# Performance work log

Measured on AMD Instinct MI355X. Metric: run time of the kernel, lower is better.

The kernel has to match this reference:

```python
import jax, jax.numpy as jnp
import numpy as np


def setup_inputs() -> dict:
    key = jax.random.key(0)
    ks = jax.random.split(key, 7)
    B, T, I, H = 32, 2048, 256, 512
    s = 1.0 / np.sqrt(H)
    return {
        "x": jax.random.normal(ks[0], (B, T, I), dtype=jnp.float32),
        "h0": jax.random.normal(ks[1], (1, B, H), dtype=jnp.float32),
        "c0": jax.random.normal(ks[2], (1, B, H), dtype=jnp.float32),
        "W_ih": jax.random.uniform(ks[3], (4 * H, I), dtype=jnp.float32, minval=-s, maxval=s),
        "W_hh": jax.random.uniform(ks[4], (4 * H, H), dtype=jnp.float32, minval=-s, maxval=s),
        "b_ih": jax.random.uniform(ks[5], (4 * H,), dtype=jnp.float32, minval=-s, maxval=s),
        "b_hh": jax.random.uniform(ks[6], (4 * H,), dtype=jnp.float32, minval=-s, maxval=s),
    }


def _lstm(x, h0, c0, W_ih, W_hh, b_ih, b_hh):
    # x: [B, T, I] (batch_first). Precompute input projections for all steps.
    H = h0.shape[-1]
    x_tf = jnp.swapaxes(x, 0, 1)                       # [T, B, I]
    x_gates = jnp.einsum("tbi,gi->tbg", x_tf, W_ih) + b_ih + b_hh  # [T, B, 4H]

    def step(carry, xg):
        h, c = carry
        gates = xg + h @ W_hh.T                        # [B, 4H]
        i_g, f_g, g_g, o_g = jnp.split(gates, 4, axis=-1)  # torch gate order i,f,g,o
        i_g = jax.nn.sigmoid(i_g)
        f_g = jax.nn.sigmoid(f_g)
        g_g = jnp.tanh(g_g)
        o_g = jax.nn.sigmoid(o_g)
        c_new = f_g * c + i_g * g_g
        h_new = o_g * jnp.tanh(c_new)
        return (h_new, c_new), h_new

    (h_f, c_f), hs = jax.lax.scan(step, (h0[0], c0[0]), x_gates)
    result = jnp.swapaxes(hs, 0, 1)                    # [B, T, H] (batch_first)
    return result, (h_f[None], c_f[None])


def reference(x, h0, c0, W_ih, W_hh, b_ih, b_hh):
    return _lstm(x, h0, c0, W_ih, W_hh, b_ih, b_hh)
```

## Files before the change

### kernel.cpp

```cpp
#include <hip/hip_runtime.h>
#include <hip/hip_bf16.h>
#include <stdint.h>


#define B_   32
#define T_   2048
#define I_   256
#define H_   512
#define NB   32
#define NTHR 512
#define JC   16
#define SA   776
#define KSTEPS 24
#define NPAIR (B_ * H_ / 2)

typedef __attribute__((ext_vector_type(8))) short short8;
typedef __attribute__((ext_vector_type(4))) float f32x4;

__device__ __forceinline__ unsigned short f2bf_bits(float v) {
    unsigned int u = __builtin_bit_cast(unsigned int, v);
    unsigned int r = (u + 0x7FFFu + ((u >> 16) & 1u)) >> 16;
    return (unsigned short)r;
}
__device__ __forceinline__ float sigm(float x) {
    return 1.0f / (1.0f + __expf(-x));
}
__device__ __forceinline__ float tanh_fast(float x) {
    float e = __expf(2.0f * x);
    return 1.0f - 2.0f / (e + 1.0f);
}

__global__ void lstm_init(const float* __restrict__ h0,
                          unsigned long long* __restrict__ hbuf0) {
    int i = blockIdx.x * 256 + threadIdx.x;
    if (i < NPAIR) {
        const int b = i >> 8;
        const int c = (i & 255) * 2;
        const unsigned lo = f2bf_bits(h0[b * H_ + c]);
        const unsigned hi = f2bf_bits(h0[b * H_ + c + 1]);
        const unsigned pair = lo | (hi << 16);
        hbuf0[i] = ((unsigned long long)pair << 32) | 0u;
    }
}

__global__ __launch_bounds__(NTHR) void lstm_persistent(
    const float* __restrict__ x,
    const float* __restrict__ c0,
    const float* __restrict__ Wih,
    const float* __restrict__ Whh,
    const float* __restrict__ bih,
    const float* __restrict__ bhh,
    float* __restrict__ out,
    unsigned long long* hbuf)
{
    __shared__ __align__(16) unsigned short Als[B_][SA];
    __shared__ float g_ls[B_][4 * JC + 1];

    const int tid  = threadIdx.x;
    const int bid  = blockIdx.x;
    const int lane = tid & 63;
    const int wave = tid >> 6;
    const int mi   = (wave & 1) * 16;
    const int q    = wave >> 1;
    const int l15  = lane & 15;
    const int kq8  = (lane >> 4) * 8;

    const int grow = q * H_ + bid * JC + l15;
    short8 bfrag[KSTEPS];
#pragma unroll
    for (int s = 0; s < KSTEPS; ++s) {
        const int k0 = s * 32 + kq8;
        short8 f;
#pragma unroll
        for (int j = 0; j < 8; ++j) {
            const int k = k0 + j;
            const float v = (k < H_) ? Whh[(size_t)grow * H_ + k]
                                     : Wih[(size_t)grow * I_ + (k - H_)];
            f[j] = (short)f2bf_bits(v);
        }
        bfrag[s] = f;
    }

    const int eb   = tid >> 4;
    const int ejj  = tid & 15;
    const int ecol = bid * JC + ejj;
    float bias_i = bih[0 * H_ + ecol] + bhh[0 * H_ + ecol];
    float bias_f = bih[1 * H_ + ecol] + bhh[1 * H_ + ecol];
    float bias_g = bih[2 * H_ + ecol] + bhh[2 * H_ + ecol];
    float bias_o = bih[3 * H_ + ecol] + bhh[3 * H_ + ecol];
    float c_reg  = c0[eb * H_ + ecol];

    for (int t = 0; t < T_; ++t) {
        float4 xv[4];
#pragma unroll
        for (int i = 0; i < 4; ++i) {
            const int idx = tid + i * NTHR;
            const int m = idx >> 6, k4 = idx & 63;
            xv[i] = *(const float4*)(x + (size_t)m * T_ * I_ +
                                     (size_t)t * I_ + k4 * 4);
        }
        asm volatile("" ::: "memory");

        const unsigned tt = (unsigned)t;
        unsigned long long* hsrc = hbuf + (size_t)(t & 1) * NPAIR;
        unsigned long long hv[16];
        unsigned need = 0xFFFFu;
        do {
#pragma unroll
            for (int i = 0; i < 16; ++i) {
                if (need & (1u << i)) {
                    hv[i] = __hip_atomic_load(&hsrc[tid + i * NTHR],
                                              __ATOMIC_RELAXED,
                                              __HIP_MEMORY_SCOPE_AGENT);
                }
            }
            unsigned ok = 0;
#pragma unroll
            for (int i = 0; i < 16; ++i)
                if ((unsigned)hv[i] == tt) ok |= (1u << i);
            need &= ~ok;
        } while (need);

#pragma unroll
        for (int i = 0; i < 16; ++i) {
            const int j = tid + i * NTHR;
            const int m = j >> 8;
            const int c = (j & 255) * 2;
            *(unsigned int*)&Als[m][c] = (unsigned int)(hv[i] >> 32);
        }
#pragma unroll
        for (int i = 0; i < 4; ++i) {
            const int idx = tid + i * NTHR;
            const int m = idx >> 6, k4 = idx & 63;
            ushort4 p;
            p.x = f2bf_bits(xv[i].x); p.y = f2bf_bits(xv[i].y);
            p.z = f2bf_bits(xv[i].z); p.w = f2bf_bits(xv[i].w);
            *(ushort4*)&Als[m][H_ + k4 * 4] = p;
        }
        __syncthreads();

        f32x4 acc = {0.f, 0.f, 0.f, 0.f};
        const int mrow = mi + l15;
#pragma unroll
        for (int s = 0; s < KSTEPS; ++s) {
            const short8 a = *(const short8*)&Als[mrow][s * 32 + kq8];
            acc = __builtin_amdgcn_mfma_f32_16x16x32_bf16(a, bfrag[s], acc, 0, 0, 0);
        }
#pragma unroll
        for (int r = 0; r < 4; ++r) {
            g_ls[mi + (lane >> 4) * 4 + r][q * JC + l15] = acc[r];
        }
        __syncthreads();

        const float pi = g_ls[eb][ejj]          + bias_i;
        const float pf = g_ls[eb][JC + ejj]     + bias_f;
        const float pg = g_ls[eb][2 * JC + ejj] + bias_g;
        const float po = g_ls[eb][3 * JC + ejj] + bias_o;
        const float ig = sigm(pi), fg = sigm(pf);
        const float gg = tanh_fast(pg), og = sigm(po);
        c_reg = fg * c_reg + ig * gg;
        const float h = og * tanh_fast(c_reg);

        const unsigned hvb = f2bf_bits(h);
        const unsigned nbv = __shfl_xor(hvb, 1);
        if ((ejj & 1) == 0) {
            const unsigned pair = hvb | (nbv << 16);
            const unsigned long long word =
                ((unsigned long long)pair << 32) | (unsigned)(t + 1);
            __hip_atomic_store(
                &hbuf[(size_t)((t + 1) & 1) * NPAIR + eb * 256 + (ecol >> 1)],
                word, __ATOMIC_RELAXED, __HIP_MEMORY_SCOPE_AGENT);
        }

        out[(size_t)eb * T_ * H_ + (size_t)t * H_ + ecol] = h;
        if (t == T_ - 1) {
            out[(size_t)B_ * T_ * H_ + eb * H_ + ecol] = h;
            out[(size_t)B_ * T_ * H_ + B_ * H_ + eb * H_ + ecol] = c_reg;
        }
    }
}

extern "C" void kernel_launch(void* const* d_in, const int* in_sizes, int n_in,
                              void* d_out, int out_size, void* d_ws, size_t ws_size,
                              hipStream_t stream) {
    const float* x   = (const float*)d_in[0];
    const float* h0  = (const float*)d_in[1];
    const float* c0  = (const float*)d_in[2];
    const float* Wih = (const float*)d_in[3];
    const float* Whh = (const float*)d_in[4];
    const float* bih = (const float*)d_in[5];
    const float* bhh = (const float*)d_in[6];
    float* out = (float*)d_out;

    unsigned long long* hbuf = (unsigned long long*)d_ws;

    hipLaunchKernelGGL(lstm_init, dim3(32), dim3(256), 0, stream, h0, hbuf);
    hipLaunchKernelGGL(lstm_persistent, dim3(NB), dim3(NTHR), 0, stream,
                       x, c0, Wih, Whh, bih, bhh, out, hbuf);
}
```

Measured before the change: 7.145 ms.

## Overlap input-projection MFMAs with h-wait and prefetch x two steps ahead

Splits the shared A tile into a recurrent h part and a double-buffered x part. The x-projection MFMAs now run before the spin-wait on the previous step's h, so input-gate work overlaps with the cross-block synchronisation, and x is prefetched and converted two timesteps ahead. Shared-memory addresses use an XOR swizzle in place of row padding to avoid bank conflicts. The second h buffer is also initialised to a sentinel. This adds a third LDS buffer and more address arithmetic in the critical loop.

```diff
diff --git a/kernel.cpp b/kernel.cpp
--- a/kernel.cpp
+++ b/kernel.cpp
@@ -10,7 +10,6 @@
 #define NB   32
 #define NTHR 512
 #define JC   16
-#define SA   776
 #define KSTEPS 24
 #define NPAIR (B_ * H_ / 2)
 
@@ -31,7 +30,7 @@
 }
 
 __global__ void lstm_init(const float* __restrict__ h0,
-                          unsigned long long* __restrict__ hbuf0) {
+                          unsigned long long* __restrict__ hbuf) {
     int i = blockIdx.x * 256 + threadIdx.x;
     if (i < NPAIR) {
         const int b = i >> 8;
@@ -39,11 +38,12 @@
         const unsigned lo = f2bf_bits(h0[b * H_ + c]);
         const unsigned hi = f2bf_bits(h0[b * H_ + c + 1]);
         const unsigned pair = lo | (hi << 16);
-        hbuf0[i] = ((unsigned long long)pair << 32) | 0u;
-    }
-}
-
-__global__ __launch_bounds__(NTHR) void lstm_persistent(
+        hbuf[i] = ((unsigned long long)pair << 32) | 0u;
+        hbuf[NPAIR + i] = 0xFFFFFFFFull;
+    }
+}
+
+__global__ __launch_bounds__(NTHR, 1) void lstm_persistent(
     const float* __restrict__ x,
     const float* __restrict__ c0,
     const float* __restrict__ Wih,
@@ -53,7 +53,8 @@
     float* __restrict__ out,
     unsigned long long* hbuf)
 {
-    __shared__ __align__(16) unsigned short Als[B_][SA];
+    __shared__ __align__(16) unsigned short Als[B_][512];
+    __shared__ __align__(16) unsigned short Axls[2][B_][256];
     __shared__ float g_ls[B_][4 * JC + 1];
 
     const int tid  = threadIdx.x;
@@ -64,6 +65,7 @@
     const int q    = wave >> 1;
     const int l15  = lane & 15;
     const int kq8  = (lane >> 4) * 8;
+    const int qv   = lane >> 4;
 
     const int grow = q * H_ + bid * JC + l15;
     short8 bfrag[KSTEPS];
@@ -90,22 +92,71 @@
     float bias_o = bih[3 * H_ + ecol] + bhh[3 * H_ + ecol];
     float c_reg  = c0[eb * H_ + ecol];
 
-    for (int t = 0; t < T_; ++t) {
-        float4 xv[4];
+    char* alsb = (char*)&Als[0][0];
+
+    float4 xv[4];
+#pragma unroll
+    for (int i = 0; i < 4; ++i) {
+        const int idx = tid + i * NTHR;
+        const int m = idx >> 6, k4 = idx & 63;
+        xv[i] = *(const float4*)(x + (size_t)m * T_ * I_ + k4 * 4);
+    }
+    {
+        char* axw = (char*)&Axls[0][0][0];
 #pragma unroll
         for (int i = 0; i < 4; ++i) {
             const int idx = tid + i * NTHR;
             const int m = idx >> 6, k4 = idx & 63;
-            xv[i] = *(const float4*)(x + (size_t)m * T_ * I_ +
-                                     (size_t)t * I_ + k4 * 4);
-        }
-        asm volatile("" ::: "memory");
-
+            ushort4 pk;
+            pk.x = f2bf_bits(xv[i].x); pk.y = f2bf_bits(xv[i].y);
+            pk.z = f2bf_bits(xv[i].z); pk.w = f2bf_bits(xv[i].w);
+            const unsigned a = (unsigned)(m * 512) +
+                (((unsigned)(k4 >> 1) ^ (unsigned)(m & 7)) << 4) +
+                (unsigned)((k4 & 1) * 8);
+            *(ushort4*)(axw + a) = pk;
+        }
+    }
+#pragma unroll
+    for (int i = 0; i < 4; ++i) {
+        const int idx = tid + i * NTHR;
+        const int m = idx >> 6, k4 = idx & 63;
+        xv[i] = *(const float4*)(x + (size_t)m * T_ * I_ + (size_t)I_ + k4 * 4);
+    }
+    __syncthreads();
+
+    const int  mrow = mi + l15;
+    const unsigned r7 = (unsigned)(mrow & 7);
+
+    for (int t = 0; t < T_; ++t) {
         const unsigned tt = (unsigned)t;
         unsigned long long* hsrc = hbuf + (size_t)(t & 1) * NPAIR;
+
         unsigned long long hv[16];
-        unsigned need = 0xFFFFu;
-        do {
+#pragma unroll
+        for (int i = 0; i < 16; ++i) {
+            hv[i] = __hip_atomic_load(&hsrc[tid + i * NTHR],
+                                      __ATOMIC_RELAXED,
+                                      __HIP_MEMORY_SCOPE_AGENT);
+        }
+        asm volatile("" ::: "memory");
+
+        f32x4 acc = {0.f, 0.f, 0.f, 0.f};
+        {
+            const char* axb = (const char*)&Axls[t & 1][0][0];
+#pragma unroll
+            for (int s = 0; s < 8; ++s) {
+                const unsigned off = (unsigned)(mrow * 512) +
+                    (((unsigned)(s * 4 + qv) ^ r7) << 4);
+                const short8 a = *(const short8*)(axb + off);
+                acc = __builtin_amdgcn_mfma_f32_16x16x32_bf16(a, bfrag[16 + s], acc, 0, 0, 0);
+            }
+        }
+
+        unsigned need = 0;
+#pragma unroll
+        for (int i = 0; i < 16; ++i)
+            if ((unsigned)hv[i] != tt) need |= (1u << i);
+        while (need) {
 #pragma unroll
             for (int i = 0; i < 16; ++i) {
                 if (need & (1u << i)) {
@@ -119,36 +170,46 @@
             for (int i = 0; i < 16; ++i)
                 if ((unsigned)hv[i] == tt) ok |= (1u << i);
             need &= ~ok;
-        } while (need);
+        }
 
 #pragma unroll
         for (int i = 0; i < 16; ++i) {
-            const int j = tid + i * NTHR;
-            const int m = j >> 8;
-            const int c = (j & 255) * 2;
-            *(unsigned int*)&Als[m][c] = (unsigned int)(hv[i] >> 32);
-        }
-#pragma unroll
-        for (int i = 0; i < 4; ++i) {
-            const int idx = tid + i * NTHR;
-            const int m = idx >> 6, k4 = idx & 63;
-            ushort4 p;
-            p.x = f2bf_bits(xv[i].x); p.y = f2bf_bits(xv[i].y);
-            p.z = f2bf_bits(xv[i].z); p.w = f2bf_bits(xv[i].w);
-            *(ushort4*)&Als[m][H_ + k4 * 4] = p;
+            const int j  = tid + i * NTHR;
+            const int m  = j >> 8;
+            const int cp = j & 255;
+            const unsigned a = (unsigned)(m * 1024) +
+                (((unsigned)(cp >> 2) ^ (unsigned)(m & 7)) << 4) +
+                (unsigned)((cp & 3) * 4);
+            *(unsigned*)(alsb + a) = (unsigned)(hv[i] >> 32);
         }
         __syncthreads();
 
-        f32x4 acc = {0.f, 0.f, 0.f, 0.f};
-        const int mrow = mi + l15;
-#pragma unroll
-        for (int s = 0; s < KSTEPS; ++s) {
-            const short8 a = *(const short8*)&Als[mrow][s * 32 + kq8];
+#pragma unroll
+        for (int s = 0; s < 16; ++s) {
+            const unsigned off = (unsigned)(mrow * 1024) +
+                (((unsigned)(s * 4 + qv) ^ r7) << 4);
+            const short8 a = *(const short8*)(alsb + off);
             acc = __builtin_amdgcn_mfma_f32_16x16x32_bf16(a, bfrag[s], acc, 0, 0, 0);
         }
 #pragma unroll
         for (int r = 0; r < 4; ++r) {
             g_ls[mi + (lane >> 4) * 4 + r][q * JC + l15] = acc[r];
+        }
+
+        {
+            char* axw = (char*)&Axls[(t + 1) & 1][0][0];
+#pragma unroll
+            for (int i = 0; i < 4; ++i) {
+                const int idx = tid + i * NTHR;
+                const int m = idx >> 6, k4 = idx & 63;
+                ushort4 pk;
+                pk.x = f2bf_bits(xv[i].x); pk.y = f2bf_bits(xv[i].y);
+                pk.z = f2bf_bits(xv[i].z); pk.w = f2bf_bits(xv[i].w);
+                const unsigned a = (unsigned)(m * 512) +
+                    (((unsigned)(k4 >> 1) ^ (unsigned)(m & 7)) << 4) +
+                    (unsigned)((k4 & 1) * 8);
+                *(ushort4*)(axw + a) = pk;
+            }
         }
         __syncthreads();
 
@@ -170,6 +231,17 @@
             __hip_atomic_store(
                 &hbuf[(size_t)((t + 1) & 1) * NPAIR + eb * 256 + (ecol >> 1)],
                 word, __ATOMIC_RELAXED, __HIP_MEMORY_SCOPE_AGENT);
+        }
+
+        {
+            const int tn = (t + 2 < T_) ? t + 2 : T_ - 1;
+#pragma unroll
+            for (int i = 0; i < 4; ++i) {
+                const int idx = tid + i * NTHR;
+                const int m = idx >> 6, k4 = idx & 63;
+                xv[i] = *(const float4*)(x + (size_t)m * T_ * I_ +
+                                         (size_t)tn * I_ + k4 * 4);
+            }
         }
 
         out[(size_t)eb * T_ * H_ + (size_t)t * H_ + ecol] = h;
```

New measurement: 10.42 ms. 45.9% more time.

## Precompute input projection in a parallel GEMM before the recurrent loop

Applied to the files above, without the earlier changes.

Adds a separate bf16 MFMA GEMM kernel that computes x·W_ih^T for all timesteps into workspace before the recurrence. The persistent recurrent kernel then only multiplies h by W_hh (16 K-steps instead of 24) and prefetches the precomputed gate inputs for the next step. This takes the x loads, bf16 conversion and input matmul off the serial critical path. In exchange it needs a large workspace buffer (~0.5 GB), falling back to the old fused kernel when the workspace is too small, and adds extra global memory traffic to write and read the precomputed gates.

```diff
diff --git a/kernel.cpp b/kernel.cpp
--- a/kernel.cpp
+++ b/kernel.cpp
@@ -10,9 +10,12 @@
 #define NB   32
 #define NTHR 512
 #define JC   16
+#define KH   16
+#define KSTEPS 24
 #define SA   776
-#define KSTEPS 24
 #define NPAIR (B_ * H_ / 2)
+#define G4H  (4 * H_)
+#define XGSTEP (B_ * G4H)
 
 typedef __attribute__((ext_vector_type(8))) short short8;
 typedef __attribute__((ext_vector_type(4))) float f32x4;
@@ -31,7 +34,8 @@
 }
 
 __global__ void lstm_init(const float* __restrict__ h0,
-                          unsigned long long* __restrict__ hbuf0) {
+                          const float* __restrict__ Wih,
+                          unsigned long long* __restrict__ ws, int big) {
     int i = blockIdx.x * 256 + threadIdx.x;
     if (i < NPAIR) {
         const int b = i >> 8;
@@ -39,19 +43,210 @@
         const unsigned lo = f2bf_bits(h0[b * H_ + c]);
         const unsigned hi = f2bf_bits(h0[b * H_ + c + 1]);
         const unsigned pair = lo | (hi << 16);
-        hbuf0[i] = ((unsigned long long)pair << 32) | 0u;
-    }
-}
-
-__global__ __launch_bounds__(NTHR) void lstm_persistent(
+        ws[i] = ((unsigned long long)pair << 32) | 0u;
+        ws[NPAIR + i] = 0xFFFFFFFFull;
+    }
+    if (big) {
+        unsigned short* Wihb = (unsigned short*)(ws + 2 * (size_t)NPAIR);
+        const int base = i * 64;
+#pragma unroll
+        for (int k = 0; k < 16; ++k) {
+            float4 v = *(const float4*)(Wih + base + k * 4);
+            ushort4 p;
+            p.x = f2bf_bits(v.x); p.y = f2bf_bits(v.y);
+            p.z = f2bf_bits(v.z); p.w = f2bf_bits(v.w);
+            *(ushort4*)(Wihb + base + k * 4) = p;
+        }
+    }
+}
+
+__global__ __launch_bounds__(NTHR) void xg_gemm(
     const float* __restrict__ x,
+    unsigned long long* __restrict__ ws)
+{
+    __shared__ __align__(16) unsigned short Axp[B_][I_];
+
+    const unsigned short* Wihb = (const unsigned short*)(ws + 2 * (size_t)NPAIR);
+    float* xg = (float*)(Wihb + (size_t)G4H * I_);
+
+    const int t    = blockIdx.x;
+    const int tid  = threadIdx.x;
+    const int lane = tid & 63;
+    const int wave = tid >> 6;
+    const int l15  = lane & 15;
+    const int kq8  = (lane >> 4) * 8;
+
+#pragma unroll
+    for (int i = 0; i < 4; ++i) {
+        const int idx = tid + i * NTHR;
+        const int m = idx >> 6, k4 = idx & 63;
+        float4 v = *(const float4*)(x + (size_t)m * T_ * I_ +
+                                    (size_t)t * I_ + k4 * 4);
+        ushort4 pk;
+        pk.x = f2bf_bits(v.x); pk.y = f2bf_bits(v.y);
+        pk.z = f2bf_bits(v.z); pk.w = f2bf_bits(v.w);
+        *(ushort4*)&Axp[m][k4 * 4] = pk;
+    }
+    __syncthreads();
+
+    short8 afr[2][8];
+#pragma unroll
+    for (int mt = 0; mt < 2; ++mt)
+#pragma unroll
+        for (int ks = 0; ks < 8; ++ks)
+            afr[mt][ks] = *(const short8*)&Axp[mt * 16 + l15][ks * 32 + kq8];
+
+    for (int j = 0; j < 16; ++j) {
+        const int n0 = (wave + 8 * j) * 16;
+        short8 bfr[8];
+#pragma unroll
+        for (int ks = 0; ks < 8; ++ks)
+            bfr[ks] = *(const short8*)(Wihb + (size_t)(n0 + l15) * I_ +
+                                       ks * 32 + kq8);
+        f32x4 a0 = {0.f,0.f,0.f,0.f}, a1 = {0.f,0.f,0.f,0.f};
+#pragma unroll
+        for (int ks = 0; ks < 8; ++ks) {
+            a0 = __builtin_amdgcn_mfma_f32_16x16x32_bf16(afr[0][ks], bfr[ks], a0, 0, 0, 0);
+            a1 = __builtin_amdgcn_mfma_f32_16x16x32_bf16(afr[1][ks], bfr[ks], a1, 0, 0, 0);
+        }
+        float* o = xg + (size_t)t * XGSTEP + n0 + l15;
+#pragma unroll
+        for (int r = 0; r < 4; ++r) {
+            o[(size_t)(((lane >> 4) * 4) + r) * G4H]      = a0[r];
+            o[(size_t)(16 + ((lane >> 4) * 4) + r) * G4H] = a1[r];
+        }
+    }
+}
+
+__global__ __launch_bounds__(NTHR, 1) void lstm_rec(
     const float* __restrict__ c0,
-    const float* __restrict__ Wih,
     const float* __restrict__ Whh,
     const float* __restrict__ bih,
     const float* __restrict__ bhh,
     float* __restrict__ out,
-    unsigned long long* hbuf)
+    unsigned long long* ws)
+{
+    __shared__ __align__(16) unsigned short Als[B_][SA];
+    __shared__ float g_ls[B_][4 * JC + 1];
+
+    const unsigned short* Wihb = (const unsigned short*)(ws + 2 * (size_t)NPAIR);
+    const float* xg = (const float*)(Wihb + (size_t)G4H * I_);
+
+    const int tid  = threadIdx.x;
+    const int bid  = blockIdx.x;
+    const int lane = tid & 63;
+    const int wave = tid >> 6;
+    const int mi   = (wave & 1) * 16;
+    const int q    = wave >> 1;
+    const int l15  = lane & 15;
+    const int kq8  = (lane >> 4) * 8;
+
+    const int grow = q * H_ + bid * JC + l15;
+    short8 bfrag[KH];
+#pragma unroll
+    for (int s = 0; s < KH; ++s) {
+        const int k0 = s * 32 + kq8;
+        short8 f;
+#pragma unroll
+        for (int j = 0; j < 8; ++j)
+            f[j] = (short)f2bf_bits(Whh[(size_t)grow * H_ + k0 + j]);
+        bfrag[s] = f;
+    }
+
+    const int eb   = tid >> 4;
+    const int ejj  = tid & 15;
+    const int ecol = bid * JC + ejj;
+    float bias_i = bih[0 * H_ + ecol] + bhh[0 * H_ + ecol];
+    float bias_f = bih[1 * H_ + ecol] + bhh[1 * H_ + ecol];
+    float bias_g = bih[2 * H_ + ecol] + bhh[2 * H_ + ecol];
+    float bias_o = bih[3 * H_ + ecol] + bhh[3 * H_ + ecol];
+    float c_reg  = c0[eb * H_ + ecol];
+
+    const float* xp0 = xg + (size_t)eb * G4H + ecol;
+    float xg0 = xp0[0], xg1 = xp0[H_], xg2 = xp0[2 * H_], xg3 = xp0[3 * H_];
+
+    for (int t = 0; t < T_; ++t) {
+        const unsigned tt = (unsigned)t;
+        unsigned long long* hsrc = ws + (size_t)(t & 1) * NPAIR;
+
+        unsigned long long hv[16];
+        unsigned need = 0xFFFFu;
+        do {
+#pragma unroll
+            for (int i = 0; i < 16; ++i) {
+                if (need & (1u << i)) {
+                    hv[i] = __hip_atomic_load(&hsrc[tid + i * NTHR],
+                                              __ATOMIC_RELAXED,
+                                              __HIP_MEMORY_SCOPE_AGENT);
+                }
+            }
+            unsigned ok = 0;
+#pragma unroll
+            for (int i = 0; i < 16; ++i)
+                if ((unsigned)hv[i] == tt) ok |= (1u << i);
+            need &= ~ok;
+        } while (need);
+
+#pragma unroll
+        for (int i = 0; i < 16; ++i) {
+            const int j = tid + i * NTHR;
+            const int m = j >> 8;
+            const int c = (j & 255) * 2;
+            *(unsigned int*)&Als[m][c] = (unsigned int)(hv[i] >> 32);
+        }
+        __syncthreads();
+
+        f32x4 acc = {0.f, 0.f, 0.f, 0.f};
+        const int mrow = mi + l15;
+#pragma unroll
+        for (int s = 0; s < KH; ++s) {
+            const short8 a = *(const short8*)&Als[mrow][s * 32 + kq8];
+            acc = __builtin_amdgcn_mfma_f32_16x16x32_bf16(a, bfrag[s], acc, 0, 0, 0);
+        }
+#pragma unroll
+        for (int r = 0; r < 4; ++r) {
+            g_ls[mi + (lane >> 4) * 4 + r][q * JC + l15] = acc[r];
+        }
+        __syncthreads();
+
+        const float pi = g_ls[eb][ejj]          + bias_i + xg0;
+        const float pf = g_ls[eb][JC + ejj]     + bias_f + xg1;
+        const float pg = g_ls[eb][2 * JC + ejj] + bias_g + xg2;
+        const float po = g_ls[eb][3 * JC + ejj] + bias_o + xg3;
+        const float ig = sigm(pi), fg = sigm(pf);
+        const float gg = tanh_fast(pg), og = sigm(po);
+        c_reg = fg * c_reg + ig * gg;
+        const float h = og * tanh_fast(c_reg);
+
+        const unsigned hvb = f2bf_bits(h);
+        const unsigned nbv = __shfl_xor(hvb, 1);
+        if ((ejj & 1) == 0) {
+            const unsigned pair = hvb | (nbv << 16);
+            const unsigned long long word =
+                ((unsigned long long)pair << 32) | (unsigned)(t + 1);
+            __hip_atomic_store(
+                &ws[(size_t)((t + 1) & 1) * NPAIR + eb * 256 + (ecol >> 1)],
+                word, __ATOMIC_RELAXED, __HIP_MEMORY_SCOPE_AGENT);
+        }
+
+        if (t + 1 < T_) {
+            const float* p = xg + (size_t)(t + 1) * XGSTEP + eb * G4H + ecol;
+            xg0 = p[0]; xg1 = p[H_]; xg2 = p[2 * H_]; xg3 = p[3 * H_];
+        }
+
+        out[(size_t)eb * T_ * H_ + (size_t)t * H_ + ecol] = h;
+        if (t == T_ - 1) {
+            out[(size_t)B_ * T_ * H_ + eb * H_ + ecol] = h;
+            out[(size_t)B_ * T_ * H_ + B_ * H_ + eb * H_ + ecol] = c_reg;
+        }
+    }
+}
+
+__global__ __launch_bounds__(NTHR) void lstm_fb(
+    const float* __restrict__ x, const float* __restrict__ c0,
+    const float* __restrict__ Wih, const float* __restrict__ Whh,
+    const float* __restrict__ bih, const float* __restrict__ bhh,
+    float* __restrict__ out, unsigned long long* hbuf)
 {
     __shared__ __align__(16) unsigned short Als[B_][SA];
     __shared__ float g_ls[B_][4 * JC + 1];
@@ -192,9 +387,21 @@
     const float* bhh = (const float*)d_in[6];
     float* out = (float*)d_out;
 
-    unsigned long long* hbuf = (unsigned long long*)d_ws;
-
-    hipLaunchKernelGGL(lstm_init, dim3(32), dim3(256), 0, stream, h0, hbuf);
-    hipLaunchKernelGGL(lstm_persistent, dim3(NB), dim3(NTHR), 0, stream,
-                       x, c0, Wih, Whh, bih, bhh, out, hbuf);
-}
+    unsigned long long* ws = (unsigned long long*)d_ws;
+
+    const size_t need = 2 * (size_t)NPAIR * 8
+                      + (size_t)G4H * I_ * 2
+                      + (size_t)T_ * XGSTEP * 4;
+    const int big = (ws_size >= need) ? 1 : 0;
+
+    hipLaunchKernelGGL(lstm_init, dim3(32), dim3(256), 0, stream,
+                       h0, Wih, ws, big);
+    if (big) {
+        hipLaunchKernelGGL(xg_gemm, dim3(T_), dim3(NTHR), 0, stream, x, ws);
+        hipLaunchKernelGGL(lstm_rec, dim3(NB), dim3(NTHR), 0, stream,
+                           c0, Whh, bih, bhh, out, ws);
+    } else {
+        hipLaunchKernelGGL(lstm_fb, dim3(NB), dim3(NTHR), 0, stream,
+                           x, c0, Wih, Whh, bih, bhh, out, ws);
+    }
+}
```

Measured after the change: 7.122 ms. About the same (-0.3%).
